# Kernel tuning notes

Measured on AMD Instinct MI355X. Metric: run time of the kernel, lower is better.

Reference implementation:

```python
import jax, jax.numpy as jnp
import numpy as np

D_MAIN = 256
D_INT = 512
N_FEAT = 128
N_CLASSES = 10
B = 1024
N_CAND = 100000
CTX = 96
EPS = 1e-5


def layer_norm(x, scale, bias):
    m = jnp.mean(x, axis=-1, keepdims=True)
    v = jnp.var(x, axis=-1, keepdims=True)
    return (x - m) / jnp.sqrt(v + EPS) * scale + bias


def setup_inputs() -> dict:
    key = jax.random.key(0)
    ks = jax.random.split(key, 16)

    def lin_w(k, fi, fo):
        return jax.random.uniform(k, (fi, fo), minval=-1.0, maxval=1.0, dtype=jnp.float32) / np.sqrt(fi)

    def lin_b(k, fi, fo):
        return jax.random.uniform(k, (fo,), minval=-1.0, maxval=1.0, dtype=jnp.float32) / np.sqrt(fi)

    return {
        "x_num": jax.random.normal(ks[0], (B, N_FEAT), dtype=jnp.float32),
        "cand_num": jax.random.normal(ks[1], (N_CAND, N_FEAT), dtype=jnp.float32),
        "cand_y": jax.random.randint(ks[2], (N_CAND,), 0, N_CLASSES),
        "context_size": CTX,
        # input linear (forward_E with encoder_n_blocks=0)
        "W_lin": lin_w(ks[3], N_FEAT, D_MAIN), "b_lin": lin_b(ks[3], N_FEAT, D_MAIN),
        # K projection
        "W_K": lin_w(ks[4], D_MAIN, D_MAIN), "b_K": lin_b(ks[4], D_MAIN, D_MAIN),
        # label embedding Y (init uniform(-1, 1) per reset_parameters)
        "Y_emb": jax.random.uniform(ks[5], (N_CLASSES, D_MAIN), minval=-1.0, maxval=1.0, dtype=jnp.float32),
        # T: Linear(d, d_int) -> ReLU -> Linear(d_int, d, bias=False)
        "T_W1": lin_w(ks[6], D_MAIN, D_INT), "T_b1": lin_b(ks[6], D_MAIN, D_INT),
        "T_W2": lin_w(ks[7], D_INT, D_MAIN),
        # predictor block (LayerNorm -> Linear -> ReLU -> Dropout -> Linear), residual
        "bp_ln_s": jnp.ones((D_MAIN,), jnp.float32), "bp_ln_b": jnp.zeros((D_MAIN,), jnp.float32),
        "bp_W1": lin_w(ks[8], D_MAIN, D_INT), "bp_b1": lin_b(ks[8], D_MAIN, D_INT),
        "bp_W2": lin_w(ks[9], D_INT, D_MAIN), "bp_b2": lin_b(ks[9], D_INT, D_MAIN),
        # head P: LayerNorm -> ReLU -> Linear(d, n_classes)
        "P_ln_s": jnp.ones((D_MAIN,), jnp.float32), "P_ln_b": jnp.zeros((D_MAIN,), jnp.float32),
        "P_W": lin_w(ks[10], D_MAIN, N_CLASSES), "P_b": lin_b(ks[10], D_MAIN, N_CLASSES),
    }


def reference(x_num, cand_num, cand_y, context_size,
              W_lin, b_lin, W_K, b_K, Y_emb, T_W1, T_b1, T_W2,
              bp_ln_s, bp_ln_b, bp_W1, bp_b1, bp_W2, bp_b2,
              P_ln_s, P_ln_b, P_W, P_b):
    # forward_E (encoder_n_blocks=0 => single Linear, normlization is None)
    x = x_num @ W_lin + b_lin                       # [B, d]
    k = x @ W_K + b_K                               # [B, d]

    # candidate keys computed under torch.no_grad in the original -> stop_gradient
    ki_all = jax.lax.stop_gradient((cand_num @ W_lin + b_lin) @ W_K + b_K)  # [N, d]

    # FAISS GpuIndexFlatL2 search: exact L2 top-k (smallest squared distance)
    d2 = (jnp.sum(k * k, axis=-1, keepdims=True)
          - 2.0 * (k @ ki_all.T)
          + jnp.sum(ki_all * ki_all, axis=-1))      # [B, N]
    _, I = jax.lax.top_k(-jax.lax.stop_gradient(d2), context_size)  # [B, C]

    ki = ki_all[I]                                  # [B, C, d]
    diff = k[:, None, :] - ki                       # [B, C, d]
    # NOTE: source computes S = -(-|k|^2 + 2 k.ki - |ki|^2) = +squared distance
    S = jnp.sum(diff * diff, axis=-1)               # [B, C]
    w = jax.nn.softmax(S, axis=-1)                  # context_dropout inactive at inference

    enc_y = Y_emb[cand_y[I]]                        # [B, C, d]
    V = enc_y + jax.nn.relu(diff @ T_W1 + T_b1) @ T_W2
    V = jnp.einsum('bc,bcd->bd', w, V)              # weighted aggregation

    x = x + V
    # predictor block (predictor_n_blocks=1)
    h = layer_norm(x, bp_ln_s, bp_ln_b)
    h = jax.nn.relu(h @ bp_W1 + bp_b1) @ bp_W2 + bp_b2
    x = x + h
    # head P
    return jax.nn.relu(layer_norm(x, P_ln_s, P_ln_b)) @ P_W + P_b
```

## Files before the change

### kernel.cpp

```cpp
#include <hip/hip_runtime.h>
#include <hip/hip_bf16.h>

#define B_ROWS   1024
#define N_FEAT   128
#define D_MAIN   256
#define D_INT    512
#define N_CAND   100000
#define CTX      96
#define N_CLS    10
#define CHN      12500
#define NREST    87500
#define RKEEP    128
#define SCAP     6144
#define MH       50000
#define SVSTRIDE 16

typedef __attribute__((ext_vector_type(8))) short bf16x8;
typedef __attribute__((ext_vector_type(4))) float f32x4;
typedef unsigned long long u64;

__device__ __forceinline__ float wsum(float v) {
    #pragma unroll
    for (int o = 32; o > 0; o >>= 1) v += __shfl_down(v, o);
    return v;
}
__device__ __forceinline__ float wmax(float v) {
    #pragma unroll
    for (int o = 32; o > 0; o >>= 1) v = fmaxf(v, __shfl_down(v, o));
    return v;
}
__device__ __forceinline__ float blockSum256(float v, float* red) {
    int t = threadIdx.x;
    float s = wsum(v);
    if ((t & 63) == 0) red[t >> 6] = s;
    __syncthreads();
    s = red[0] + red[1] + red[2] + red[3];
    __syncthreads();
    return s;
}
__device__ __forceinline__ float b2f(unsigned short u) {
    return __uint_as_float(((unsigned)u) << 16);
}
__device__ __forceinline__ unsigned short f2b(float f) {
    unsigned x = __float_as_uint(f);
    return (unsigned short)((x + 0x7fff + ((x >> 16) & 1)) >> 16);
}
__device__ __forceinline__ unsigned fkey(float f) {
    unsigned u = __float_as_uint(f);
    return u ^ ((((int)u >> 31)) | 0x80000000u);
}
__device__ __forceinline__ float finv(unsigned k) {
    unsigned u = (k & 0x80000000u) ? (k ^ 0x80000000u) : ~k;
    return __uint_as_float(u);
}
#define SPLIT1(x, hv, lv) { unsigned short _h = f2b(x); hv = (short)_h; lv = (short)f2b((x) - b2f(_h)); }

__global__ __launch_bounds__(256) void encode_batch(
    const float* __restrict__ xn, const float* __restrict__ Wl, const float* __restrict__ bl,
    const float* __restrict__ Wk, const float* __restrict__ bk,
    float* __restrict__ xout, float* __restrict__ kout, float* __restrict__ knorm)
{
    int b = blockIdx.x, t = threadIdx.x;
    __shared__ float si[128], sx[256], red[4];
    if (t < 128) si[t] = xn[b * N_FEAT + t];
    __syncthreads();
    float a = bl[t];
    for (int i = 0; i < 128; ++i) a += si[i] * Wl[i * D_MAIN + t];
    xout[b * D_MAIN + t] = a;
    sx[t] = a;
    __syncthreads();
    float a2 = bk[t];
    for (int i = 0; i < 256; ++i) a2 += sx[i] * Wk[i * D_MAIN + t];
    kout[b * D_MAIN + t] = a2;
    float s = blockSum256(a2 * a2, red);
    if (t == 0) knorm[b] = s;
}

template<bool WRITE_BF16>
__global__ __launch_bounds__(256) void gemm_split3(
    const float* __restrict__ A,
    const unsigned short* __restrict__ Bh,
    const unsigned short* __restrict__ Bl,
    const float* __restrict__ bias,
    float* __restrict__ Cf,
    unsigned short* __restrict__ Cbf,
    int M, int N, int K)
{
    __shared__ __align__(16) short Ash[4096], Asl[4096], Bsh[4096], Bsl[4096];
    const int t = threadIdx.x;
    const int bm = blockIdx.x * 128, bn = blockIdx.y * 128;
    const int wave = t >> 6, lane = t & 63;
    const int wm = (wave >> 1) * 64, wn = (wave & 1) * 64;
    const int lr = lane & 15, lkg = lane >> 4;
    f32x4 acc[4][4] = {};
    const int row0 = t >> 2, kg0 = t & 3;
    const int row1 = row0 + 64;
    const int p0 = ((kg0 + (row0 >> 2)) & 3) ^ (row0 & 3);
    const int p1 = ((kg0 + (row1 >> 2)) & 3) ^ (row1 & 3);
    const int gm0 = bm + row0, gm1 = bm + row1;
    const int n0r = bn + row0, n1r = bn + row1;

    float4 u00, u01, u10, u11;
    bf16x8 b0h, b0l, b1h, b1l;
    auto prefetch = [&](int kq) {
        float4 z4 = make_float4(0.f, 0.f, 0.f, 0.f); bf16x8 z = {};
        u00 = z4; u01 = z4; u10 = z4; u11 = z4;
        b0h = z; b0l = z; b1h = z; b1l = z;
        if (gm0 < M) {
            const float* ap = A + (size_t)gm0 * K + kq + kg0 * 8;
            u00 = *(const float4*)ap; u01 = *(const float4*)(ap + 4);
        }
        if (gm1 < M) {
            const float* ap = A + (size_t)gm1 * K + kq + kg0 * 8;
            u10 = *(const float4*)ap; u11 = *(const float4*)(ap + 4);
        }
        if (n0r < N) {
            b0h = *(const bf16x8*)(Bh + (size_t)n0r * K + kq + kg0 * 8);
            b0l = *(const bf16x8*)(Bl + (size_t)n0r * K + kq + kg0 * 8);
        }
        if (n1r < N) {
            b1h = *(const bf16x8*)(Bh + (size_t)n1r * K + kq + kg0 * 8);
            b1l = *(const bf16x8*)(Bl + (size_t)n1r * K + kq + kg0 * 8);
        }
    };
    prefetch(0);

    for (int k0 = 0; k0 < K; k0 += 32) {
        bf16x8 a0h, a0l, a1h, a1l;
        SPLIT1(u00.x, a0h[0], a0l[0]); SPLIT1(u00.y, a0h[1], a0l[1]);
        SPLIT1(u00.z, a0h[2], a0l[2]); SPLIT1(u00.w, a0h[3], a0l[3]);
        SPLIT1(u01.x, a0h[4], a0l[4]); SPLIT1(u01.y, a0h[5], a0l[5]);
        SPLIT1(u01.z, a0h[6], a0l[6]); SPLIT1(u01.w, a0h[7], a0l[7]);
        SPLIT1(u10.x, a1h[0], a1l[0]); SPLIT1(u10.y, a1h[1], a1l[1]);
        SPLIT1(u10.z, a1h[2], a1l[2]); SPLIT1(u10.w, a1h[3], a1l[3]);
        SPLIT1(u11.x, a1h[4], a1l[4]); SPLIT1(u11.y, a1h[5], a1l[5]);
        SPLIT1(u11.z, a1h[6], a1l[6]); SPLIT1(u11.w, a1h[7], a1l[7]);
        __syncthreads();
        *(bf16x8*)&Ash[(row0 * 4 + p0) * 8] = a0h;
        *(bf16x8*)&Asl[(row0 * 4 + p0) * 8] = a0l;
        *(bf16x8*)&Ash[(row1 * 4 + p1) * 8] = a1h;
        *(bf16x8*)&Asl[(row1 * 4 + p1) * 8] = a1l;
        *(bf16x8*)&Bsh[(row0 * 4 + p0) * 8] = b0h;
        *(bf16x8*)&Bsl[(row0 * 4 + p0) * 8] = b0l;
        *(bf16x8*)&Bsh[(row1 * 4 + p1) * 8] = b1h;
        *(bf16x8*)&Bsl[(row1 * 4 + p1) * 8] = b1l;
        if (k0 + 32 < K) prefetch(k0 + 32);
        __syncthreads();
        bf16x8 ah[4], al[4], bh[4], blo[4];
        #pragma unroll
        for (int m = 0; m < 4; ++m) {
            int r = wm + m * 16 + lr;
            int p = ((lkg + (r >> 2)) & 3) ^ (r & 3);
            ah[m] = *(const bf16x8*)&Ash[(r * 4 + p) * 8];
            al[m] = *(const bf16x8*)&Asl[(r * 4 + p) * 8];
        }
        #pragma unroll
        for (int n = 0; n < 4; ++n) {
            int r = wn + n * 16 + lr;
            int p = ((lkg + (r >> 2)) & 3) ^ (r & 3);
            bh[n] = *(const bf16x8*)&Bsh[(r * 4 + p) * 8];
            blo[n] = *(const bf16x8*)&Bsl[(r * 4 + p) * 8];
        }
        #pragma unroll
        for (int m = 0; m < 4; ++m)
            #pragma unroll
            for (int n = 0; n < 4; ++n) {
                acc[m][n] = __builtin_amdgcn_mfma_f32_16x16x32_bf16(al[m], bh[n], acc[m][n], 0, 0, 0);
                acc[m][n] = __builtin_amdgcn_mfma_f32_16x16x32_bf16(ah[m], blo[n], acc[m][n], 0, 0, 0);
                acc[m][n] = __builtin_amdgcn_mfma_f32_16x16x32_bf16(ah[m], bh[n], acc[m][n], 0, 0, 0);
            }
    }
    #pragma unroll
    for (int m = 0; m < 4; ++m) {
        #pragma unroll
        for (int n = 0; n < 4; ++n) {
            f32x4 a = acc[m][n];
            int gcol = bn + wn + n * 16 + lr;
            if (gcol >= N) continue;
            float bv = bias[gcol];
            #pragma unroll
            for (int r = 0; r < 4; ++r) {
                int grow = bm + wm + m * 16 + lkg * 4 + r;
                if (grow >= M) continue;
                float v = a[r] + bv;
                Cf[(size_t)grow * N + gcol] = v;
                if (WRITE_BF16) Cbf[(size_t)grow * N + gcol] = f2b(v);
            }
        }
    }
}

template<bool RELU, bool OUT_BF16, int MODE>
__global__ __launch_bounds__(256) void gemm_bf16(
    const unsigned short* __restrict__ A,
    const unsigned short* __restrict__ Bt,
    const float* __restrict__ bias,
    void* __restrict__ C, int M, int N, int K,
    const float* __restrict__ knrm,
    const unsigned* __restrict__ tau32, int* __restrict__ svcnt,
    u64* __restrict__ surv, int n0)
{
    __shared__ __align__(16) short As[4096];
    __shared__ __align__(16) short Bs[4096];
    const int t = threadIdx.x;
    const int bm = blockIdx.x * 128, bn = blockIdx.y * 128;
    const int wave = t >> 6, lane = t & 63;
    const int wm = (wave >> 1) * 64, wn = (wave & 1) * 64;
    const int lr = lane & 15, lkg = lane >> 4;
    f32x4 acc[4][4] = {};
    const int row0 = t >> 2, kg0 = t & 3;
    const int row1 = row0 + 64;
    const int p0 = ((kg0 + (row0 >> 2)) & 3) ^ (row0 & 3);
    const int p1 = ((kg0 + (row1 >> 2)) & 3) ^ (row1 & 3);
    const int gm0 = bm + row0, gm1 = bm + row1;
    const int n0r = bn + row0, n1r = bn + row1;

    bf16x8 a0, a1, b0, b1;
    auto prefetch = [&](int kq) {
        bf16x8 z = {};
        a0 = z; a1 = z; b0 = z; b1 = z;
        if (gm0 < M) a0 = *(const bf16x8*)(A + (size_t)gm0 * K + kq + kg0 * 8);
        if (gm1 < M) a1 = *(const bf16x8*)(A + (size_t)gm1 * K + kq + kg0 * 8);
        if (n0r < N) b0 = *(const bf16x8*)(Bt + (size_t)n0r * K + kq + kg0 * 8);
        if (n1r < N) b1 = *(const bf16x8*)(Bt + (size_t)n1r * K + kq + kg0 * 8);
    };
    prefetch(0);

    for (int k0 = 0; k0 < K; k0 += 32) {
        __syncthreads();
        *(bf16x8*)&As[(row0 * 4 + p0) * 8] = a0;
        *(bf16x8*)&As[(row1 * 4 + p1) * 8] = a1;
        *(bf16x8*)&Bs[(row0 * 4 + p0) * 8] = b0;
        *(bf16x8*)&Bs[(row1 * 4 + p1) * 8] = b1;
        if (k0 + 32 < K) prefetch(k0 + 32);
        __syncthreads();
        bf16x8 af[4], bfr[4];
        #pragma unroll
        for (int m = 0; m < 4; ++m) {
            int r = wm + m * 16 + lr;
            int p = ((lkg + (r >> 2)) & 3) ^ (r & 3);
            af[m] = *(const bf16x8*)&As[(r * 4 + p) * 8];
        }
        #pragma unroll
        for (int n = 0; n < 4; ++n) {
            int r = wn + n * 16 + lr;
            int p = ((lkg + (r >> 2)) & 3) ^ (r & 3);
            bfr[n] = *(const bf16x8*)&Bs[(r * 4 + p) * 8];
        }
        #pragma unroll
        for (int m = 0; m < 4; ++m)
            #pragma unroll
            for (int n = 0; n < 4; ++n)
                acc[m][n] = __builtin_amdgcn_mfma_f32_16x16x32_bf16(
                    af[m], bfr[n], acc[m][n], 0, 0, 0);
    }
    if (MODE == 2) {
        unsigned taur[16];
        #pragma unroll
        for (int m = 0; m < 4; ++m)
            #pragma unroll
            for (int r = 0; r < 4; ++r)
                taur[m * 4 + r] = tau32[bm + wm + m * 16 + lkg * 4 + r];
        float knv[4];
        #pragma unroll
        for (int n = 0; n < 4; ++n) {
            int gcol = bn + wn + n * 16 + lr;
            knv[n] = (gcol < N) ? knrm[gcol] : 0.f;
        }
        #pragma unroll
        for (int m = 0; m < 4; ++m) {
            #pragma unroll
            for (int r = 0; r < 4; ++r) {
                int grow = bm + wm + m * 16 + lkg * 4 + r;
                #pragma unroll
                for (int n = 0; n < 4; ++n) {
                    int gcol = bn + wn + n * 16 + lr;
                    bool pass = false;
                    unsigned key = 0;
                    if (gcol < N) {
                        key = fkey(knv[n] - 2.0f * acc[m][n][r]);
                        pass = key <= taur[m * 4 + r];
                    }
                    u64 bal = __ballot(pass);
                    unsigned g16 = (unsigned)((bal >> (lkg * 16)) & 0xFFFFu);
                    if (g16) {
                        int cntp = __popc(g16);
                        int first = __ffs(g16) - 1;
                        int base = 0;
                        if (lr == first) base = atomicAdd(&svcnt[grow * SVSTRIDE], cntp);
                        base = __shfl(base, lkg * 16 + first);
                        if (pass) {
                            int p = base + __popc(g16 & ((1u << lr) - 1u));
                            if (p < SCAP)
                                surv[(size_t)grow * SCAP + p] =
                                    ((u64)key << 32) | (unsigned)(n0 + gcol);
                        }
                    }
                }
            }
        }
        return;
    }
    #pragma unroll
    for (int m = 0; m < 4; ++m) {
        #pragma unroll
        for (int n = 0; n < 4; ++n) {
            f32x4 a = acc[m][n];
            int gcol = bn + wn + n * 16 + lr;
            if (gcol >= N) continue;
            float bv = (MODE == 0 && bias) ? bias[gcol] : 0.f;
            float kn = (MODE == 1) ? knrm[gcol] : 0.f;
            #pragma unroll
            for (int r = 0; r < 4; ++r) {
                int grow = bm + wm + m * 16 + lkg * 4 + r;
                if (grow >= M) continue;
                if (MODE == 1) {
                    ((float*)C)[(size_t)grow * N + gcol] = kn - 2.0f * a[r];
                } else {
                    float v = a[r] + bv;
                    if (RELU) v = fmaxf(v, 0.f);
                    if (OUT_BF16)
                        ((unsigned short*)C)[(size_t)grow * N + gcol] = f2b(v);
                    else
                        ((float*)C)[(size_t)grow * N + gcol] = v;
                }
            }
        }
    }
}

__global__ __launch_bounds__(256) void cvt_f32_bf16_vec(
    const float* __restrict__ in, unsigned short* __restrict__ out, int n4)
{
    int i = blockIdx.x * 256 + threadIdx.x;
    if (i >= n4) return;
    float4 v = ((const float4*)in)[i];
    ushort4 u;
    u.x = f2b(v.x); u.y = f2b(v.y); u.z = f2b(v.z); u.w = f2b(v.w);
    ((ushort4*)out)[i] = u;
}
__global__ __launch_bounds__(256) void cvt_transpose(
    const float* __restrict__ W, unsigned short* __restrict__ Wt, int K, int N)
{
    int idx = blockIdx.x * 256 + threadIdx.x;
    if (idx >= K * N) return;
    int k = idx / N, n = idx % N;
    Wt[(size_t)n * K + k] = f2b(W[idx]);
}
__global__ __launch_bounds__(256) void cvt_split_transpose(
    const float* __restrict__ W, unsigned short* __restrict__ Wh,
    unsigned short* __restrict__ Wl, int K, int N)
{
    int idx = blockIdx.x * 256 + threadIdx.x;
    if (idx >= K * N) return;
    int k = idx / N, n = idx % N;
    float v = W[idx];
    unsigned short h = f2b(v);
    Wh[(size_t)n * K + k] = h;
    Wl[(size_t)n * K + k] = f2b(v - b2f(h));
}

__global__ __launch_bounds__(256) void rownorms(const float* __restrict__ ki,
                                                float* __restrict__ out, int M)
{
    int n = blockIdx.x * 4 + (threadIdx.x >> 6);
    int lane = threadIdx.x & 63;
    if (n >= M) return;
    float4 v = *(const float4*)(ki + (size_t)n * D_MAIN + lane * 4);
    float s = v.x * v.x + v.y * v.y + v.z * v.z + v.w * v.w;
    s = wsum(s);
    if (lane == 0) out[n] = s;
}

__device__ void bitonic512(u64* s, int t)
{
    for (int k = 2; k <= 512; k <<= 1) {
        for (int j = k >> 1; j > 0; j >>= 1) {
            __syncthreads();
            #pragma unroll
            for (int q = 0; q < 2; ++q) {
                int l = t + q * 256;
                int p = l ^ j;
                if (p > l) {
                    u64 a = s[l], bb = s[p];
                    bool up = ((l & k) == 0);
                    if ((a > bb) == up) { s[l] = bb; s[p] = a; }
                }
            }
        }
    }
    __syncthreads();
}
__device__ void bitonic1024(u64* s, int t)
{
    for (int k = 2; k <= 1024; k <<= 1) {
        for (int j = k >> 1; j > 0; j >>= 1) {
            __syncthreads();
            #pragma unroll
            for (int q = 0; q < 4; ++q) {
                int l = t + q * 256;
                int p = l ^ j;
                if (p > l) {
                    u64 a = s[l], bb = s[p];
                    bool up = ((l & k) == 0);
                    if ((a > bb) == up) { s[l] = bb; s[p] = a; }
                }
            }
        }
    }
    __syncthreads();
}

__global__ __launch_bounds__(256) void pilot_select(
    const float* __restrict__ scores, u64* __restrict__ pilotbuf,
    unsigned* __restrict__ tau32)
{
    int b = blockIdx.x, t = threadIdx.x;
    int lane = t & 63;
    __shared__ u64 s[1024];
    __shared__ int cnt;
    __shared__ u64 tauf;
    const float* row = scores + (size_t)b * CHN;
    #pragma unroll
    for (int q = 0; q < 4; ++q) {
        int n = t + q * 256;
        s[n] = ((u64)fkey(row[n]) << 32) | (unsigned)n;
    }
    __syncthreads();
    bitonic1024(s, t);
    if (t == 0) { cnt = 128; tauf = s[127]; }
    #pragma unroll
    for (int q = 0; q < 4; ++q) { int n = t + q * 256; if (n >= 128) s[n] = ~0ULL; }
    __syncthreads();
    for (int base = 1024; base < CHN; base += 1024) {
        u64 tau = tauf;
        int n = base + t * 4;
        float4 v = make_float4(0.f, 0.f, 0.f, 0.f);
        bool inb = (n < CHN);
        if (inb) v = *(const float4*)(row + n);
        #pragma unroll
        for (int j = 0; j < 4; ++j) {
            float x = (&v.x)[j];
            u64 e = inb ? (((u64)fkey(x) << 32) | (unsigned)(n + j)) : ~0ULL;
            bool pass = e < tau;
            u64 m = __ballot(pass);
            if (m) {
                int bs = 0;
                if (lane == 0) bs = atomicAdd(&cnt, (int)__popcll(m));
                bs = __shfl(bs, 0);
                if (pass) {
                    int p = bs + (int)__popcll(m & ((1ULL << lane) - 1ULL));
                    if (p < 1024) s[p] = e;
                }
            }
        }
        __syncthreads();
        if (cnt > 512) {
            bitonic1024(s, t);
            if (t == 0) { cnt = 128; tauf = s[127]; }
            #pragma unroll
            for (int q = 0; q < 4; ++q) { int n2 = t + q * 256; if (n2 >= 128) s[n2] = ~0ULL; }
        }
        __syncthreads();
    }
    bitonic1024(s, t);
    if (t < 128) pilotbuf[(size_t)b * 128 + t] = s[t];
    if (t == 0) tau32[b] = (unsigned)(s[127] >> 32);
}

__global__ __launch_bounds__(128) void init_surv(
    const u64* __restrict__ pilotbuf, u64* __restrict__ surv, int* __restrict__ svcnt)
{
    int b = blockIdx.x, t = threadIdx.x;
    surv[(size_t)b * SCAP + t] = pilotbuf[(size_t)b * 128 + t];
    if (t == 0) svcnt[b * SVSTRIDE] = 128;
}

__global__ __launch_bounds__(256) void final_select(
    const u64* __restrict__ surv, const int* __restrict__ svcnt,
    int* __restrict__ refI)
{
    int b = blockIdx.x, t = threadIdx.x;
    int lane = t & 63;
    __shared__ u64 s[1024];
    __shared__ int cnt;
    __shared__ u64 tauf;
    int total = svcnt[b * SVSTRIDE]; if (total > SCAP) total = SCAP;
    const u64* rowp = surv + (size_t)b * SCAP;
    #pragma unroll
    for (int q = 0; q < 4; ++q) {
        int n = t + q * 256;
        s[n] = (n < total) ? rowp[n] : ~0ULL;
    }
    __syncthreads();
    bitonic1024(s, t);
    if (t == 0) { cnt = 128; tauf = s[127]; }
    #pragma unroll
    for (int q = 0; q < 4; ++q) { int n = t + q * 256; if (n >= 128) s[n] = ~0ULL; }
    __syncthreads();
    for (int base = 1024; base < total; base += 1024) {
        u64 tau = tauf;
        int n = base + t * 4;
        #pragma unroll
        for (int j = 0; j < 4; ++j) {
            u64 e = (n + j < total) ? rowp[n + j] : ~0ULL;
            bool pass = e < tau;
            u64 m = __ballot(pass);
            if (m) {
                int bs = 0;
                if (lane == 0) bs = atomicAdd(&cnt, (int)__popcll(m));
                bs = __shfl(bs, 0);
                if (pass) {
                    int p = bs + (int)__popcll(m & ((1ULL << lane) - 1ULL));
                    if (p < 1024) s[p] = e;
                }
            }
        }
        __syncthreads();
        if (cnt > 512) {
            bitonic1024(s, t);
            if (t == 0) { cnt = 128; tauf = s[127]; }
            #pragma unroll
            for (int q = 0; q < 4; ++q) { int n2 = t + q * 256; if (n2 >= 128) s[n2] = ~0ULL; }
        }
        __syncthreads();
    }
    bitonic1024(s, t);
    if (t < RKEEP) refI[b * RKEEP + t] = (int)(unsigned)(s[t] & 0xffffffffULL);
}

__global__ __launch_bounds__(256) void refine(
    const float* __restrict__ kmat, const float* __restrict__ kiall,
    const float* __restrict__ knorm, const float* __restrict__ kinorm,
    const int* __restrict__ refI, int* __restrict__ Ifin, float* __restrict__ Sbuf)
{
    int b = blockIdx.x, t = threadIdx.x;
    int w = t >> 6, lane = t & 63;
    __shared__ float kk[256];
    __shared__ u64 s[512];
    kk[t] = kmat[b * D_MAIN + t];
    s[t] = ~0ULL; s[t + 256] = ~0ULL;
    __syncthreads();
    float kn = knorm[b];
    for (int sv = w; sv < RKEEP; sv += 4) {
        int n = refI[b * RKEEP + sv];
        float4 a = *(const float4*)&kk[lane * 4];
        float4 bb = ((const float4*)(kiall + (size_t)n * D_MAIN))[lane];
        float d = a.x * bb.x + a.y * bb.y + a.z * bb.z + a.w * bb.w;
        d = wsum(d);
        if (lane == 0) {
            float d2 = kn + kinorm[n] - 2.f * d;
            s[sv] = ((u64)fkey(d2) << 32) | (unsigned)n;
        }
    }
    __syncthreads();
    bitonic512(s, t);
    if (t < CTX) {
        u64 e = s[t];
        Ifin[b * CTX + t] = (int)(unsigned)(e & 0xffffffffULL);
        Sbuf[b * CTX + t] = finv((unsigned)(e >> 32));
    }
}

__global__ __launch_bounds__(64) void gather_diff_bf(
    const float* __restrict__ kmat, const float* __restrict__ kiall,
    const int* __restrict__ I, unsigned short* __restrict__ diffb)
{
    int bc = blockIdx.x;
    int b = bc / CTX;
    int t = threadIdx.x;
    int idx = I[bc];
    float4 kv = ((const float4*)(kmat + (size_t)b * D_MAIN))[t];
    float4 iv = ((const float4*)(kiall + (size_t)idx * D_MAIN))[t];
    ushort4 u;
    u.x = f2b(kv.x - iv.x); u.y = f2b(kv.y - iv.y);
    u.z = f2b(kv.z - iv.z); u.w = f2b(kv.w - iv.w);
    ((ushort4*)(diffb + (size_t)bc * D_MAIN))[t] = u;
}

__global__ __launch_bounds__(128) void softmax96(const float* __restrict__ S,
                                                 float* __restrict__ w)
{
    int b = blockIdx.x, t = threadIdx.x;
    __shared__ float rm[2], rs[2];
    float v = (t < CTX) ? S[b * CTX + t] : -__builtin_inff();
    float m = wmax(v);
    if ((t & 63) == 0) rm[t >> 6] = m;
    __syncthreads();
    m = fmaxf(rm[0], rm[1]);
    float e = (t < CTX) ? expf(v - m) : 0.f;
    float ss = wsum(e);
    if ((t & 63) == 0) rs[t >> 6] = ss;
    __syncthreads();
    float Z = rs[0] + rs[1];
    if (t < CTX) w[b * CTX + t] = e / Z;
}

__global__ __launch_bounds__(256) void aggregate(
    const float* __restrict__ w, const int* __restrict__ I,
    const int* __restrict__ cand_y, const float* __restrict__ Yemb,
    const float* __restrict__ mlp, const float* __restrict__ x,
    float* __restrict__ x2)
{
    int b = blockIdx.x, t = threadIdx.x;
    __shared__ float ws[CTX];
    __shared__ int lab[CTX];
    if (t < CTX) {
        ws[t] = w[b * CTX + t];
        lab[t] = cand_y[I[b * CTX + t]];
    }
    __syncthreads();
    float acc = 0.f;
    for (int c = 0; c < CTX; ++c) {
        acc += ws[c] * (Yemb[lab[c] * D_MAIN + t] + mlp[((size_t)b * CTX + c) * D_MAIN + t]);
    }
    x2[b * D_MAIN + t] = x[b * D_MAIN + t] + acc;
}

__global__ __launch_bounds__(256) void predictor_head(
    const float* __restrict__ x2,
    const float* __restrict__ lns, const float* __restrict__ lnb,
    const float* __restrict__ W1, const float* __restrict__ b1,
    const float* __restrict__ W2, const float* __restrict__ b2,
    const float* __restrict__ plns, const float* __restrict__ plnb,
    const float* __restrict__ PW, const float* __restrict__ Pb,
    float* __restrict__ out)
{
    int b = blockIdx.x, t = threadIdx.x;
    __shared__ float ln1[256], hdn[512], red[4];
    float xv = x2[b * D_MAIN + t];
    float s1 = blockSum256(xv, red);
    float s2 = blockSum256(xv * xv, red);
    float mean = s1 * (1.f / 256.f);
    float var = s2 * (1.f / 256.f) - mean * mean;
    float rstd = rsqrtf(var + 1e-5f);
    ln1[t] = (xv - mean) * rstd * lns[t] + lnb[t];
    __syncthreads();
    #pragma unroll
    for (int rep = 0; rep < 2; ++rep) {
        int j = t + rep * 256;
        float a = b1[j];
        for (int i = 0; i < 256; ++i) a += ln1[i] * W1[i * D_INT + j];
        hdn[j] = fmaxf(a, 0.f);
    }
    __syncthreads();
    float a3 = b2[t];
    for (int i = 0; i < 512; ++i) a3 += hdn[i] * W2[i * D_MAIN + t];
    float x3 = xv + a3;
    float s3 = blockSum256(x3, red);
    float s4 = blockSum256(x3 * x3, red);
    float m2 = s3 * (1.f / 256.f);
    float v2 = s4 * (1.f / 256.f) - m2 * m2;
    float r2 = rsqrtf(v2 + 1e-5f);
    float rv = fmaxf((x3 - m2) * r2 * plns[t] + plnb[t], 0.f);
    __syncthreads();
    ln1[t] = rv;
    __syncthreads();
    if (t < N_CLS) {
        float a = Pb[t];
        for (int i = 0; i < 256; ++i) a += ln1[i] * PW[i * N_CLS + t];
        out[b * N_CLS + t] = a;
    }
}

extern "C" void kernel_launch(void* const* d_in, const int* in_sizes, int n_in,
                              void* d_out, int out_size, void* d_ws, size_t ws_size,
                              hipStream_t stream)
{
    (void)in_sizes; (void)n_in; (void)out_size; (void)ws_size;
    const float* x_num   = (const float*)d_in[0];
    const float* cand    = (const float*)d_in[1];
    const int*   cand_y  = (const int*)d_in[2];
    const float* W_lin   = (const float*)d_in[4];
    const float* b_lin   = (const float*)d_in[5];
    const float* W_K     = (const float*)d_in[6];
    const float* b_K     = (const float*)d_in[7];
    const float* Y_emb   = (const float*)d_in[8];
    const float* T_W1    = (const float*)d_in[9];
    const float* T_b1    = (const float*)d_in[10];
    const float* T_W2    = (const float*)d_in[11];
    const float* bp_ln_s = (const float*)d_in[12];
    const float* bp_ln_b = (const float*)d_in[13];
    const float* bp_W1   = (const float*)d_in[14];
    const float* bp_b1   = (const float*)d_in[15];
    const float* bp_W2   = (const float*)d_in[16];
    const float* bp_b2   = (const float*)d_in[17];
    const float* P_ln_s  = (const float*)d_in[18];
    const float* P_ln_b  = (const float*)d_in[19];
    const float* P_W     = (const float*)d_in[20];
    const float* P_b     = (const float*)d_in[21];
    float* outp = (float*)d_out;

    char* ws = (char*)d_ws;
    float* kiall  = (float*)(ws + 0);
    unsigned short* hidden = (unsigned short*)(ws + 0);
    unsigned short* ki_bf = (unsigned short*)(ws + 102400000);
    unsigned short* diffb = (unsigned short*)(ws + 102400000);
    float* mlpbuf = (float*)(ws + 102400000);
    float* hcand  = (float*)(ws + 153600000);
    float* scores = (float*)(ws + 153600000);
    u64*   surv   = (u64*)(ws + 153600000);
    const size_t T = 204800000;
    float* xbuf   = (float*)(ws + T + 0);
    float* kbuf   = (float*)(ws + T + 1048576);
    float* x2buf  = (float*)(ws + T + 2097152);
    float* knorm  = (float*)(ws + T + 3145728);
    float* kinorm = (float*)(ws + T + 3149824);
    unsigned short* k_bf = (unsigned short*)(ws + T + 3551232);
    unsigned short* Wlh  = (unsigned short*)(ws + T + 4075520);
    unsigned short* Wll  = (unsigned short*)(ws + T + 4141056);
    unsigned short* Wkh  = (unsigned short*)(ws + T + 4206592);
    unsigned short* Wkl  = (unsigned short*)(ws + T + 4337664);
    unsigned short* W1t  = (unsigned short*)(ws + T + 4468736);
    unsigned short* W2t  = (unsigned short*)(ws + T + 4730880);
    float* Sbuf   = (float*)(ws + T + 4993024);
    float* wbuf   = (float*)(ws + T + 5386240);
    int*   refI   = (int*)(ws + T + 5779456);
    int*   Ifin   = (int*)(ws + T + 6303744);
    u64*   pilotbuf = (u64*)(ws + T + 6696960);
    unsigned* tau32 = (unsigned*)(ws + T + 7745536);
    int*   svcnt  = (int*)(ws + T + 7749632);

    encode_batch<<<B_ROWS, 256, 0, stream>>>(x_num, W_lin, b_lin, W_K, b_K,
                                             xbuf, kbuf, knorm);
    cvt_split_transpose<<<128, 256, 0, stream>>>(W_lin, Wlh, Wll, N_FEAT, D_MAIN);
    cvt_split_transpose<<<256, 256, 0, stream>>>(W_K, Wkh, Wkl, D_MAIN, D_MAIN);
    cvt_transpose<<<512, 256, 0, stream>>>(T_W1, W1t, D_MAIN, D_INT);
    cvt_transpose<<<512, 256, 0, stream>>>(T_W2, W2t, D_INT, D_MAIN);
    cvt_f32_bf16_vec<<<256, 256, 0, stream>>>(kbuf, k_bf, B_ROWS * D_MAIN / 4);
    for (int h = 0; h < 2; ++h) {
        gemm_split3<false><<<dim3(391, 2), 256, 0, stream>>>(
            cand + (size_t)h * MH * N_FEAT, Wlh, Wll, b_lin,
            hcand, nullptr, MH, D_MAIN, N_FEAT);
        gemm_split3<true><<<dim3(391, 2), 256, 0, stream>>>(
            hcand, Wkh, Wkl, b_K,
            kiall + (size_t)h * MH * D_MAIN, ki_bf + (size_t)h * MH * D_MAIN,
            MH, D_MAIN, D_MAIN);
    }
    rownorms<<<25000, 256, 0, stream>>>(kiall, kinorm, N_CAND);
    gemm_bf16<false, false, 1><<<dim3(8, 98), 256, 0, stream>>>(
        k_bf, ki_bf, nullptr, scores, B_ROWS, CHN, D_MAIN, kinorm,
        nullptr, nullptr, nullptr, 0);
    pilot_select<<<B_ROWS, 256, 0, stream>>>(scores, pilotbuf, tau32);
    init_surv<<<B_ROWS, 128, 0, stream>>>(pilotbuf, surv, svcnt);
    gemm_bf16<false, false, 2><<<dim3(8, 684), 256, 0, stream>>>(
        k_bf, ki_bf + (size_t)CHN * D_MAIN, nullptr, nullptr,
        B_ROWS, NREST, D_MAIN, kinorm + CHN, tau32, svcnt, surv, CHN);
    final_select<<<B_ROWS, 256, 0, stream>>>(surv, svcnt, refI);
    refine<<<B_ROWS, 256, 0, stream>>>(kbuf, kiall, knorm, kinorm, refI, Ifin, Sbuf);
    softmax96<<<B_ROWS, 128, 0, stream>>>(Sbuf, wbuf);
    gather_diff_bf<<<B_ROWS * CTX, 64, 0, stream>>>(kbuf, kiall, Ifin, diffb);
    gemm_bf16<true, true, 0><<<dim3(768, 4), 256, 0, stream>>>(
        diffb, W1t, T_b1, hidden, B_ROWS * CTX, D_INT, D_MAIN,
        nullptr, nullptr, nullptr, nullptr, 0);
    gemm_bf16<false, false, 0><<<dim3(768, 2), 256, 0, stream>>>(
        hidden, W2t, nullptr, mlpbuf, B_ROWS * CTX, D_MAIN, D_INT,
        nullptr, nullptr, nullptr, nullptr, 0);
    aggregate<<<B_ROWS, 256, 0, stream>>>(wbuf, Ifin, cand_y, Y_emb, mlpbuf,
                                          xbuf, x2buf);
    predictor_head<<<B_ROWS, 256, 0, stream>>>(x2buf, bp_ln_s, bp_ln_b,
                                               bp_W1, bp_b1, bp_W2, bp_b2,
                                               P_ln_s, P_ln_b, P_W, P_b, outp);
}
```

Before: 970.1 us.

## Add candidate-stationary screening GEMM with full-K B tile in LDS

Replaces the generic tiled GEMM used for distance screening with a dedicated kernel. Each block loads a 128-candidate by full-K (256) tile of candidate keys into LDS once, then loops over all 1024 query rows, reading A fragments straight from global memory. The pilot chunk also shrinks from 12500 to 8192 candidates, which drops the pilot bounds checks and shifts more work to the thresholded pass. The aim is to stop re-reading candidate tiles for every query tile and to remove the per-K-step LDS staging of A. The risks are lower occupancy from 64KB of LDS per block, uncached global loads of A in the inner loop, and a looser threshold from the smaller pilot, which could let more survivors through.

```diff
diff --git a/kernel.cpp b/kernel.cpp
--- a/kernel.cpp
+++ b/kernel.cpp
@@ -8,8 +8,9 @@
 #define N_CAND   100000
 #define CTX      96
 #define N_CLS    10
-#define CHN      12500
-#define NREST    87500
+#define PCHN     8192
+#define N2       91808
+#define NB2      718
 #define RKEEP    128
 #define SCAP     6144
 #define MH       50000
@@ -190,15 +191,12 @@
     }
 }
 
-template<bool RELU, bool OUT_BF16, int MODE>
+template<bool RELU, bool OUT_BF16>
 __global__ __launch_bounds__(256) void gemm_bf16(
     const unsigned short* __restrict__ A,
     const unsigned short* __restrict__ Bt,
     const float* __restrict__ bias,
-    void* __restrict__ C, int M, int N, int K,
-    const float* __restrict__ knrm,
-    const unsigned* __restrict__ tau32, int* __restrict__ svcnt,
-    u64* __restrict__ surv, int n0)
+    void* __restrict__ C, int M, int N, int K)
 {
     __shared__ __align__(16) short As[4096];
     __shared__ __align__(16) short Bs[4096];
@@ -254,53 +252,6 @@
                 acc[m][n] = __builtin_amdgcn_mfma_f32_16x16x32_bf16(
                     af[m], bfr[n], acc[m][n], 0, 0, 0);
     }
-    if (MODE == 2) {
-        unsigned taur[16];
-        #pragma unroll
-        for (int m = 0; m < 4; ++m)
-            #pragma unroll
-            for (int r = 0; r < 4; ++r)
-                taur[m * 4 + r] = tau32[bm + wm + m * 16 + lkg * 4 + r];
-        float knv[4];
-        #pragma unroll
-        for (int n = 0; n < 4; ++n) {
-            int gcol = bn + wn + n * 16 + lr;
-            knv[n] = (gcol < N) ? knrm[gcol] : 0.f;
-        }
-        #pragma unroll
-        for (int m = 0; m < 4; ++m) {
-            #pragma unroll
-            for (int r = 0; r < 4; ++r) {
-                int grow = bm + wm + m * 16 + lkg * 4 + r;
-                #pragma unroll
-                for (int n = 0; n < 4; ++n) {
-                    int gcol = bn + wn + n * 16 + lr;
-                    bool pass = false;
-                    unsigned key = 0;
-                    if (gcol < N) {
-                        key = fkey(knv[n] - 2.0f * acc[m][n][r]);
-                        pass = key <= taur[m * 4 + r];
-                    }
-                    u64 bal = __ballot(pass);
-                    unsigned g16 = (unsigned)((bal >> (lkg * 16)) & 0xFFFFu);
-                    if (g16) {
-                        int cntp = __popc(g16);
-                        int first = __ffs(g16) - 1;
-                        int base = 0;
-                        if (lr == first) base = atomicAdd(&svcnt[grow * SVSTRIDE], cntp);
-                        base = __shfl(base, lkg * 16 + first);
-                        if (pass) {
-                            int p = base + __popc(g16 & ((1u << lr) - 1u));
-                            if (p < SCAP)
-                                surv[(size_t)grow * SCAP + p] =
-                                    ((u64)key << 32) | (unsigned)(n0 + gcol);
-                        }
-                    }
-                }
-            }
-        }
-        return;
-    }
     #pragma unroll
     for (int m = 0; m < 4; ++m) {
         #pragma unroll
@@ -308,21 +259,134 @@
             f32x4 a = acc[m][n];
             int gcol = bn + wn + n * 16 + lr;
             if (gcol >= N) continue;
-            float bv = (MODE == 0 && bias) ? bias[gcol] : 0.f;
-            float kn = (MODE == 1) ? knrm[gcol] : 0.f;
+            float bv = bias ? bias[gcol] : 0.f;
             #pragma unroll
             for (int r = 0; r < 4; ++r) {
                 int grow = bm + wm + m * 16 + lkg * 4 + r;
                 if (grow >= M) continue;
-                if (MODE == 1) {
-                    ((float*)C)[(size_t)grow * N + gcol] = kn - 2.0f * a[r];
-                } else {
-                    float v = a[r] + bv;
-                    if (RELU) v = fmaxf(v, 0.f);
-                    if (OUT_BF16)
-                        ((unsigned short*)C)[(size_t)grow * N + gcol] = f2b(v);
-                    else
-                        ((float*)C)[(size_t)grow * N + gcol] = v;
+                float v = a[r] + bv;
+                if (RELU) v = fmaxf(v, 0.f);
+                if (OUT_BF16)
+                    ((unsigned short*)C)[(size_t)grow * N + gcol] = f2b(v);
+                else
+                    ((float*)C)[(size_t)grow * N + gcol] = v;
+            }
+        }
+    }
+}
+
+template<int MODE>
+__global__ __launch_bounds__(256) void screen_gemm(
+    const unsigned short* __restrict__ A,
+    const unsigned short* __restrict__ Bt,
+    float* __restrict__ scores,
+    int N, int n0,
+    const float* __restrict__ knrm,
+    const unsigned* __restrict__ tau32, int* __restrict__ svcnt,
+    u64* __restrict__ surv)
+{
+    __shared__ __align__(16) short Bs[32768];
+    const int t = threadIdx.x;
+    const int bn = blockIdx.x * 128;
+    const int wave = t >> 6, lane = t & 63;
+    const int wm = (wave >> 1) * 64, wn = (wave & 1) * 64;
+    const int lr = lane & 15, lkg = lane >> 4;
+
+    #pragma unroll
+    for (int i = 0; i < 16; ++i) {
+        int u = t + i * 256;
+        int row = u >> 5;
+        int kg32 = u & 31;
+        int ks = kg32 >> 2, kg = kg32 & 3;
+        bf16x8 v = {};
+        int gn = bn + row;
+        if (gn < N) v = *(const bf16x8*)(Bt + (size_t)gn * D_MAIN + kg32 * 8);
+        int p = ((kg + (row >> 2)) & 3) ^ (row & 3);
+        *(bf16x8*)&Bs[((ks * 128 + row) * 4 + p) * 8] = v;
+    }
+    __syncthreads();
+
+    float knv[4];
+    #pragma unroll
+    for (int n = 0; n < 4; ++n) {
+        int gcol = bn + wn + n * 16 + lr;
+        knv[n] = (gcol < N) ? knrm[gcol] : 0.f;
+    }
+
+    for (int mt = 0; mt < 8; ++mt) {
+        f32x4 acc[4][4] = {};
+        #pragma unroll
+        for (int ks = 0; ks < 8; ++ks) {
+            bf16x8 af[4], bfr[4];
+            #pragma unroll
+            for (int m = 0; m < 4; ++m) {
+                int ar = mt * 128 + wm + m * 16 + lr;
+                af[m] = *(const bf16x8*)(A + (size_t)ar * D_MAIN + ks * 32 + lkg * 8);
+            }
+            #pragma unroll
+            for (int n = 0; n < 4; ++n) {
+                int r = wn + n * 16 + lr;
+                int p = ((lkg + (r >> 2)) & 3) ^ (r & 3);
+                bfr[n] = *(const bf16x8*)&Bs[((ks * 128 + r) * 4 + p) * 8];
+            }
+            #pragma unroll
+            for (int m = 0; m < 4; ++m)
+                #pragma unroll
+                for (int n = 0; n < 4; ++n)
+                    acc[m][n] = __builtin_amdgcn_mfma_f32_16x16x32_bf16(
+                        af[m], bfr[n], acc[m][n], 0, 0, 0);
+        }
+        if (MODE == 1) {
+            #pragma unroll
+            for (int m = 0; m < 4; ++m) {
+                #pragma unroll
+                for (int n = 0; n < 4; ++n) {
+                    int gcol = bn + wn + n * 16 + lr;
+                    if (gcol >= N) continue;
+                    #pragma unroll
+                    for (int r = 0; r < 4; ++r) {
+                        int grow = mt * 128 + wm + m * 16 + lkg * 4 + r;
+                        scores[(size_t)grow * PCHN + gcol] = knv[n] - 2.0f * acc[m][n][r];
+                    }
+                }
+            }
+        } else {
+            unsigned taur[16];
+            #pragma unroll
+            for (int m = 0; m < 4; ++m)
+                #pragma unroll
+                for (int r = 0; r < 4; ++r)
+                    taur[m * 4 + r] = tau32[mt * 128 + wm + m * 16 + lkg * 4 + r];
+            #pragma unroll
+            for (int m = 0; m < 4; ++m) {
+                #pragma unroll
+                for (int r = 0; r < 4; ++r) {
+                    int grow = mt * 128 + wm + m * 16 + lkg * 4 + r;
+                    #pragma unroll
+                    for (int n = 0; n < 4; ++n) {
+                        int gcol = bn + wn + n * 16 + lr;
+                        bool pass = false;
+                        unsigned key = 0;
+                        if (gcol < N) {
+                            key = fkey(knv[n] - 2.0f * acc[m][n][r]);
+                            pass = key <= taur[m * 4 + r];
+                        }
+                        u64 bal = __ballot(pass);
+                        unsigned g16 = (unsigned)((bal >> (lkg * 16)) & 0xFFFFu);
+                        if (g16) {
+                            int cntp = __popc(g16);
+                            int first = __ffs(g16) - 1;
+                            int base = 0;
+                            if (lr == first) base = atomicAdd(&svcnt[grow * SVSTRIDE], cntp);
+                            base = __shfl(base, lkg * 16 + first);
+                            if (pass) {
+                                int p = base + __popc(g16 & ((1u << lr) - 1u));
+                                if (p < SCAP)
+                                    surv[(size_t)grow * SCAP + p] =
+                                        ((u64)key << 32) | (unsigned)(n0 + gcol);
+                            }
+                        }
+                    }
                 }
             }
         }
@@ -420,7 +484,7 @@
     __shared__ u64 s[1024];
     __shared__ int cnt;
     __shared__ u64 tauf;
-    const float* row = scores + (size_t)b * CHN;
+    const float* row = scores + (size_t)b * PCHN;
     #pragma unroll
     for (int q = 0; q < 4; ++q) {
         int n = t + q * 256;
@@ -432,16 +496,14 @@
     #pragma unroll
     for (int q = 0; q < 4; ++q) { int n = t + q * 256; if (n >= 128) s[n] = ~0ULL; }
     __syncthreads();
-    for (int base = 1024; base < CHN; base += 1024) {
+    for (int base = 1024; base < PCHN; base += 1024) {
         u64 tau = tauf;
         int n = base + t * 4;
-        float4 v = make_float4(0.f, 0.f, 0.f, 0.f);
-        bool inb = (n < CHN);
-        if (inb) v = *(const float4*)(row + n);
+        float4 v = *(const float4*)(row + n);
         #pragma unroll
         for (int j = 0; j < 4; ++j) {
             float x = (&v.x)[j];
-            u64 e = inb ? (((u64)fkey(x) << 32) | (unsigned)(n + j)) : ~0ULL;
+            u64 e = ((u64)fkey(x) << 32) | (unsigned)(n + j);
             bool pass = e < tau;
             u64 m = __ballot(pass);
             if (m) {
@@ -738,24 +800,21 @@
             MH, D_MAIN, D_MAIN);
     }
     rownorms<<<25000, 256, 0, stream>>>(kiall, kinorm, N_CAND);
-    gemm_bf16<false, false, 1><<<dim3(8, 98), 256, 0, stream>>>(
-        k_bf, ki_bf, nullptr, scores, B_ROWS, CHN, D_MAIN, kinorm,
-        nullptr, nullptr, nullptr, 0);
+    screen_gemm<1><<<PCHN / 128, 256, 0, stream>>>(
+        k_bf, ki_bf, scores, PCHN, 0, kinorm, nullptr, nullptr, nullptr);
     pilot_select<<<B_ROWS, 256, 0, stream>>>(scores, pilotbuf, tau32);
     init_surv<<<B_ROWS, 128, 0, stream>>>(pilotbuf, surv, svcnt);
-    gemm_bf16<false, false, 2><<<dim3(8, 684), 256, 0, stream>>>(
-        k_bf, ki_bf + (size_t)CHN * D_MAIN, nullptr, nullptr,
-        B_ROWS, NREST, D_MAIN, kinorm + CHN, tau32, svcnt, surv, CHN);
+    screen_gemm<2><<<NB2, 256, 0, stream>>>(
+        k_bf, ki_bf + (size_t)PCHN * D_MAIN, nullptr, N2, PCHN,
+        kinorm + PCHN, tau32, svcnt, surv);
     final_select<<<B_ROWS, 256, 0, stream>>>(surv, svcnt, refI);
     refine<<<B_ROWS, 256, 0, stream>>>(kbuf, kiall, knorm, kinorm, refI, Ifin, Sbuf);
     softmax96<<<B_ROWS, 128, 0, stream>>>(Sbuf, wbuf);
     gather_diff_bf<<<B_ROWS * CTX, 64, 0, stream>>>(kbuf, kiall, Ifin, diffb);
-    gemm_bf16<true, true, 0><<<dim3(768, 4), 256, 0, stream>>>(
-        diffb, W1t, T_b1, hidden, B_ROWS * CTX, D_INT, D_MAIN,
-        nullptr, nullptr, nullptr, nullptr, 0);
-    gemm_bf16<false, false, 0><<<dim3(768, 2), 256, 0, stream>>>(
-        hidden, W2t, nullptr, mlpbuf, B_ROWS * CTX, D_MAIN, D_INT,
-        nullptr, nullptr, nullptr, nullptr, 0);
+    gemm_bf16<true, true><<<dim3(768, 4), 256, 0, stream>>>(
+        diffb, W1t, T_b1, hidden, B_ROWS * CTX, D_INT, D_MAIN);
+    gemm_bf16<false, false><<<dim3(768, 2), 256, 0, stream>>>(
+        hidden, W2t, nullptr, mlpbuf, B_ROWS * CTX, D_MAIN, D_INT);
     aggregate<<<B_ROWS, 256, 0, stream>>>(wbuf, Ifin, cand_y, Y_emb, mlpbuf,
                                           xbuf, x2buf);
     predictor_head<<<B_ROWS, 256, 0, stream>>>(x2buf, bp_ln_s, bp_ln_b,
```

Result: slower. 1.197 ms (+23.4%).
